# Performance work log

Hardware: AMD Instinct MI355X
Metric: run time of the kernel (lower is better)

Reference implementation:

```python
import jax, jax.numpy as jnp
import numpy as np

LOG2 = 0.6931471805599453  # shifted_softplus(x) = softplus(x) - log(2)
NUM_MOL = 20_000  # static maxm for segment reduction


def ssp(x):
    return jax.nn.softplus(x) - LOG2


def setup_inputs() -> dict:
    key = jax.random.key(0)
    ks = jax.random.split(key, 5)
    N, D, H, E, M = 1_000_000, 128, 64, 4, NUM_MOL
    x = jax.random.normal(ks[0], (N, D), dtype=jnp.float32)
    zidx = jax.random.randint(ks[1], (N,), 0, E, dtype=jnp.int32)
    idx_m = jnp.sort(jax.random.randint(ks[2], (N,), 0, M, dtype=jnp.int32))
    # stacked per-element pyramidal MLP params: D -> D//2 -> 1
    W1 = jax.random.normal(ks[3], (E, D, H), dtype=jnp.float32) * (1.0 / np.sqrt(D))
    b1 = jnp.zeros((E, H), dtype=jnp.float32)
    W2 = jax.random.normal(ks[4], (E, H, 1), dtype=jnp.float32) * (1.0 / np.sqrt(H))
    b2 = jnp.zeros((E, 1), dtype=jnp.float32)
    return dict(x=x, zidx=zidx, idx_m=idx_m, W1=W1, b1=b1, W2=W2, b2=b2)


def reference(x, zidx, idx_m, W1, b1, W2, b2):
    # ElementwiseMLP: run each element's 2-layer MLP, select per atom by element.
    E = W1.shape[0]
    yi = jnp.zeros((x.shape[0], W2.shape[-1]), dtype=x.dtype)  # [N, n_out]
    for e in range(E):  # small fixed element set
        h = ssp(x @ W1[e] + b1[e])            # [N, H]
        ye = h @ W2[e] + b2[e]                # [N, n_out]
        yi = yi + jnp.where((zidx == e)[:, None], ye, jnp.zeros((), dtype=x.dtype))
    # aggregation_mode == 'sum': index_add per molecule
    y = jax.ops.segment_sum(yi, idx_m, num_segments=NUM_MOL)  # [M, n_out]
    return jnp.squeeze(y, -1)  # [M]
```

## Files before the change

kernel.cpp:

```cpp
#include <hip/hip_runtime.h>

typedef _Float16 half8 __attribute__((ext_vector_type(8)));
typedef float f32x4 __attribute__((ext_vector_type(4)));

#define WS_COUNT(e)  ((e) * 32)
#define WS_AOFF(e)   (128 + (e))
#define WS_FILL(e)   (136 + (e))
#define WS_CUR(e)    (160 + (e) * 32)
#define WS_PERM      512

__global__ void k_count(const int* __restrict__ zidx, int N, int* __restrict__ ws) {
  __shared__ int lh[4];
  if (threadIdx.x < 4) lh[threadIdx.x] = 0;
  __syncthreads();
  const int i = blockIdx.x * 256 + threadIdx.x;
  const int z = (i < N) ? zidx[i] : -1;
  const int lane = threadIdx.x & 63;
#pragma unroll
  for (int e = 0; e < 4; ++e) {
    unsigned long long m = __ballot(z == e);
    if (lane == 0 && m) atomicAdd(&lh[e], __popcll(m));
  }
  __syncthreads();
  if (threadIdx.x < 4 && lh[threadIdx.x])
    atomicAdd(&ws[WS_COUNT(threadIdx.x)], lh[threadIdx.x]);
}

__global__ void k_offsets(int* __restrict__ ws) {
  if (threadIdx.x != 0) return;
  int off = 0;
#pragma unroll
  for (int e = 0; e < 4; ++e) {
    int c = ws[WS_COUNT(e)];
    ws[WS_AOFF(e)] = off;
    ws[WS_FILL(e)] = off + c;
    ws[WS_CUR(e)] = off;
    off += (c + 255) & ~255;
  }
  ws[WS_AOFF(4)] = off;
}

__global__ void k_scatter(const int* __restrict__ zidx, int N, int* __restrict__ ws) {
  __shared__ int wcnt[4][4];
  __shared__ int wbase[4][4];
  const int tid = threadIdx.x;
  const int lane = tid & 63;
  const int wave = tid >> 6;
  const int i = blockIdx.x * 256 + tid;
  const int z = (i < N) ? zidx[i] : -1;
  const unsigned long long m0 = __ballot(z == 0);
  const unsigned long long m1 = __ballot(z == 1);
  const unsigned long long m2 = __ballot(z == 2);
  const unsigned long long m3 = __ballot(z == 3);
  if (lane == 0) {
    wcnt[wave][0] = __popcll(m0);
    wcnt[wave][1] = __popcll(m1);
    wcnt[wave][2] = __popcll(m2);
    wcnt[wave][3] = __popcll(m3);
  }
  __syncthreads();
  if (tid < 4) {
    const int e = tid;
    const int c0 = wcnt[0][e], c1 = wcnt[1][e], c2 = wcnt[2][e], c3 = wcnt[3][e];
    const int base = atomicAdd(&ws[WS_CUR(e)], c0 + c1 + c2 + c3);
    wbase[0][e] = base;
    wbase[1][e] = base + c0;
    wbase[2][e] = base + c0 + c1;
    wbase[3][e] = base + c0 + c1 + c2;
  }
  __syncthreads();
  if (z >= 0) {
    const unsigned long long below = (1ull << lane) - 1ull;
    int r, b;
    if (z == 0)      { r = __popcll(m0 & below); b = wbase[wave][0]; }
    else if (z == 1) { r = __popcll(m1 & below); b = wbase[wave][1]; }
    else if (z == 2) { r = __popcll(m2 & below); b = wbase[wave][2]; }
    else             { r = __popcll(m3 & below); b = wbase[wave][3]; }
    ws[WS_PERM + b + r] = i;
  }
}

__global__ __launch_bounds__(256, 3)
void elemental_sorted_kernel(const float* __restrict__ x,
                             const int* __restrict__ idx_m,
                             const float* __restrict__ W1,
                             const float* __restrict__ b1,
                             const float* __restrict__ W2,
                             const float* __restrict__ b2,
                             const int* __restrict__ ws,
                             float* __restrict__ y) {
  __shared__ _Float16 w1t[8192];

  const int bstart = blockIdx.x << 8;
  if (bstart >= ws[WS_AOFF(4)]) return;
  int e = 0;
  if (bstart >= ws[WS_AOFF(1)]) e = 1;
  if (bstart >= ws[WS_AOFF(2)]) e = 2;
  if (bstart >= ws[WS_AOFF(3)]) e = 3;
  const int fillE = ws[WS_FILL(e)];

  const float* w1e = W1 + (size_t)e * 8192;
  const int tid = threadIdx.x;
#pragma unroll
  for (int t = 0; t < 4; ++t) {
    const int ch = tid + t * 256;
    const int kt = ch >> 8;
    const int nt = (ch >> 6) & 3;
    const int l2 = ch & 63;
    const int h = nt * 16 + (l2 & 15);
    const int d0 = kt * 32 + (l2 >> 4) * 8;
    half8 hv;
#pragma unroll
    for (int j = 0; j < 8; ++j)
      hv[j] = (_Float16)w1e[(d0 + j) * 64 + h];
    *(half8*)&w1t[ch * 8] = hv;
  }
  __syncthreads();

  const int lane = tid & 63;
  const int wave = tid >> 6;
  const int c = lane & 15;
  const int q = lane >> 4;
  const int pos = bstart + wave * 64 + lane;
  const int ap = (pos < fillE) ? ws[WS_PERM + pos] : -1;
  const int iv = (ap >= 0) ? idx_m[ap] : 0;

  half8 af[4][4];
#pragma unroll
  for (int mt = 0; mt < 4; ++mt) {
    int pa = __shfl(ap, mt * 16 + c);
    const f32x4* rp = (const f32x4*)(x + (long)(pa < 0 ? 0 : pa) * 128);
#pragma unroll
    for (int kt = 0; kt < 4; ++kt) {
      f32x4 u0 = rp[kt * 8 + q * 2];
      f32x4 u1 = rp[kt * 8 + q * 2 + 1];
      half8 a;
      a[0] = (_Float16)u0[0]; a[1] = (_Float16)u0[1];
      a[2] = (_Float16)u0[2]; a[3] = (_Float16)u0[3];
      a[4] = (_Float16)u1[0]; a[5] = (_Float16)u1[1];
      a[6] = (_Float16)u1[2]; a[7] = (_Float16)u1[3];
      af[mt][kt] = a;
    }
  }

  f32x4 acc[4][4];
#pragma unroll
  for (int mt = 0; mt < 4; ++mt)
#pragma unroll
    for (int nt = 0; nt < 4; ++nt)
      acc[mt][nt] = (f32x4){0.f, 0.f, 0.f, 0.f};

#pragma unroll
  for (int kt = 0; kt < 4; ++kt)
#pragma unroll
    for (int nt = 0; nt < 4; ++nt) {
      half8 bf = *(const half8*)&w1t[((kt * 4 + nt) * 64 + lane) * 8];
#pragma unroll
      for (int mt = 0; mt < 4; ++mt)
        acc[mt][nt] = __builtin_amdgcn_mfma_f32_16x16x32_f16(af[mt][kt], bf, acc[mt][nt], 0, 0, 0);
    }

  float b1v[4], w2v[4];
#pragma unroll
  for (int nt = 0; nt < 4; ++nt) {
    b1v[nt] = b1[e * 64 + nt * 16 + c];
    w2v[nt] = W2[e * 64 + nt * 16 + c];
  }
  const float b2e = b2[e];
#pragma unroll
  for (int mt = 0; mt < 4; ++mt) {
#pragma unroll
    for (int i = 0; i < 4; ++i) {
      float s = 0.0f;
#pragma unroll
      for (int nt = 0; nt < 4; ++nt) {
        float tv = acc[mt][nt][i] + b1v[nt];
        float hsp = __logf(1.0f + __expf(tv)) - 0.69314718056f;
        s = fmaf(hsp, w2v[nt], s);
      }
      s += __shfl_xor(s, 1);
      s += __shfl_xor(s, 2);
      s += __shfl_xor(s, 4);
      s += __shfl_xor(s, 8);
      const int mloc = mt * 16 + q * 4 + i;
      const int av = __shfl(ap, mloc);
      const int im = __shfl(iv, mloc);
      if (c == 0 && av >= 0)
        atomicAdd(&y[im], s + b2e);
    }
  }
}

#define LDSROW_OLD 136

__global__ __launch_bounds__(256, 2)
void elemental_atomwise_kernel(const float* __restrict__ x,
                               const int* __restrict__ zidx,
                               const int* __restrict__ idx_m,
                               const float* __restrict__ W1,
                               const float* __restrict__ b1,
                               const float* __restrict__ W2,
                               const float* __restrict__ b2,
                               float* __restrict__ y,
                               int N) {
  extern __shared__ _Float16 w1t[];
#pragma unroll
  for (int it = 0; it < 32; ++it) {
    int idx4 = threadIdx.x + it * 256;
    f32x4 v = ((const f32x4*)W1)[idx4];
    int lin = idx4 << 2;
    int d = (lin >> 6) & 127;
    int ee = lin >> 13;
    int h = lin & 63;
    int n = ee * 64 + h;
#pragma unroll
    for (int j = 0; j < 4; ++j)
      w1t[(n + j) * LDSROW_OLD + d] = (_Float16)v[j];
  }
  __syncthreads();

  const int lane = threadIdx.x & 63;
  const int wave = threadIdx.x >> 6;
  const int c = lane & 15;
  const int q = lane >> 4;
  const long tile = (long)blockIdx.x * 4 + wave;
  const long base = tile * 64;
  if (base >= N) return;

  int ameta = (base + lane < N) ? (int)(base + lane) : (N - 1);
  const int zvec = zidx[ameta];
  const int ivec = idx_m[ameta];

  half8 af[4][4];
#pragma unroll
  for (int mt = 0; mt < 4; ++mt) {
    long row = base + mt * 16 + c;
    if (row >= N) row = N - 1;
    const f32x4* rp = (const f32x4*)(x + row * 128);
#pragma unroll
    for (int kt = 0; kt < 4; ++kt) {
      f32x4 u0 = rp[kt * 8 + q * 2];
      f32x4 u1 = rp[kt * 8 + q * 2 + 1];
      half8 a;
      a[0] = (_Float16)u0[0]; a[1] = (_Float16)u0[1];
      a[2] = (_Float16)u0[2]; a[3] = (_Float16)u0[3];
      a[4] = (_Float16)u1[0]; a[5] = (_Float16)u1[1];
      a[6] = (_Float16)u1[2]; a[7] = (_Float16)u1[3];
      af[mt][kt] = a;
    }
  }

#pragma unroll
  for (int e = 0; e < 4; ++e) {
    f32x4 acc[4][4];
#pragma unroll
    for (int mt = 0; mt < 4; ++mt)
#pragma unroll
      for (int nt = 0; nt < 4; ++nt)
        acc[mt][nt] = (f32x4){0.f, 0.f, 0.f, 0.f};

#pragma unroll
    for (int kt = 0; kt < 4; ++kt) {
#pragma unroll
      for (int nt = 0; nt < 4; ++nt) {
        half8 bf = *(const half8*)&w1t[(e * 64 + nt * 16 + c) * LDSROW_OLD + kt * 32 + q * 8];
#pragma unroll
        for (int mt = 0; mt < 4; ++mt)
          acc[mt][nt] = __builtin_amdgcn_mfma_f32_16x16x32_f16(af[mt][kt], bf, acc[mt][nt], 0, 0, 0);
      }
    }

    float b1v[4], w2v[4];
#pragma unroll
    for (int nt = 0; nt < 4; ++nt) {
      b1v[nt] = b1[e * 64 + nt * 16 + c];
      w2v[nt] = W2[e * 64 + nt * 16 + c];
    }
    const float b2e = b2[e];
#pragma unroll
    for (int mt = 0; mt < 4; ++mt) {
#pragma unroll
      for (int i = 0; i < 4; ++i) {
        float s = 0.0f;
#pragma unroll
        for (int nt = 0; nt < 4; ++nt) {
          float tv = acc[mt][nt][i] + b1v[nt];
          float hsp = __logf(1.0f + __expf(tv)) - 0.69314718056f;
          s = fmaf(hsp, w2v[nt], s);
        }
        s += __shfl_xor(s, 1);
        s += __shfl_xor(s, 2);
        s += __shfl_xor(s, 4);
        s += __shfl_xor(s, 8);
        int mloc = mt * 16 + q * 4 + i;
        int zm = __shfl(zvec, mloc);
        int im = __shfl(ivec, mloc);
        if (c == 0 && zm == e && base + mloc < N)
          atomicAdd(&y[im], s + b2e);
      }
    }
  }
}

extern "C" void kernel_launch(void* const* d_in, const int* in_sizes, int n_in,
                              void* d_out, int out_size, void* d_ws, size_t ws_size,
                              hipStream_t stream) {
  const float* x = (const float*)d_in[0];
  const int* zidx = (const int*)d_in[1];
  const int* idx_m = (const int*)d_in[2];
  const float* W1 = (const float*)d_in[3];
  const float* b1 = (const float*)d_in[4];
  const float* W2 = (const float*)d_in[5];
  const float* b2 = (const float*)d_in[6];
  float* y = (float*)d_out;

  const int N = in_sizes[0] / 128;

  hipMemsetAsync(d_out, 0, (size_t)out_size * sizeof(float), stream);

  const size_t ws_need = (size_t)(WS_PERM + N + 1024) * sizeof(int);
  if (ws_size >= ws_need) {
    int* ws = (int*)d_ws;
    hipMemsetAsync(d_ws, 0, 1024, stream);
    const int nb = (N + 255) / 256;
    k_count<<<nb, 256, 0, stream>>>(zidx, N, ws);
    k_offsets<<<1, 64, 0, stream>>>(ws);
    k_scatter<<<nb, 256, 0, stream>>>(zidx, N, ws);
    const int nb4 = (N + 1020 + 255) / 256;
    elemental_sorted_kernel<<<nb4, 256, 0, stream>>>(x, idx_m, W1, b1, W2, b2, ws, y);
  } else {
    const int tiles = (N + 63) / 64;
    const int blocks = (tiles + 3) / 4;
    const size_t lds_bytes = 256 * LDSROW_OLD * sizeof(_Float16);
    elemental_atomwise_kernel<<<blocks, 256, lds_bytes, stream>>>(
        x, zidx, idx_m, W1, b1, W2, b2, y, N);
  }
}
```

Baseline: 779.9 us.

## Pre-convert W1 to fp16 once and shrink sorted kernel to 64-atom blocks

The per-element W1 fp16 conversion and MFMA-fragment swizzle move into the counting kernel, which writes them once to workspace. The sorted MLP kernel then does a straight vectorised copy into LDS instead of strided fp32 loads and conversions. Each wave now handles 16 atoms instead of 64, so each block covers 64 atoms. This cuts accumulator and fragment registers, raises the occupancy target, and gives more blocks in flight to hide the latency of the gathered x loads. In exchange, 16KB of W1 is copied into LDS per 64 atoms instead of per 256, which raises L2 and LDS traffic per atom.

```diff
diff --git a/kernel.cpp b/kernel.cpp
--- a/kernel.cpp
+++ b/kernel.cpp
@@ -9,7 +9,8 @@
 #define WS_CUR(e)    (160 + (e) * 32)
 #define WS_PERM      512
 
-__global__ void k_count(const int* __restrict__ zidx, int N, int* __restrict__ ws) {
+__global__ void k_count(const int* __restrict__ zidx, int N, int* __restrict__ ws,
+                        const float* __restrict__ W1, _Float16* __restrict__ w1h) {
   __shared__ int lh[4];
   if (threadIdx.x < 4) lh[threadIdx.x] = 0;
   __syncthreads();
@@ -20,6 +21,18 @@
   for (int e = 0; e < 4; ++e) {
     unsigned long long m = __ballot(z == e);
     if (lane == 0 && m) atomicAdd(&lh[e], __popcll(m));
+  }
+  if (blockIdx.x < 16) {
+    const int cg = blockIdx.x * 256 + threadIdx.x;
+    const int e = cg >> 10, ch = cg & 1023;
+    const int kt = ch >> 8, nt = (ch >> 6) & 3, l2 = ch & 63;
+    const int h = nt * 16 + (l2 & 15);
+    const int d0 = kt * 32 + (l2 >> 4) * 8;
+    const float* w1e = W1 + (size_t)e * 8192;
+    half8 hv;
+#pragma unroll
+    for (int j = 0; j < 8; ++j) hv[j] = (_Float16)w1e[(d0 + j) * 64 + h];
+    *(half8*)&w1h[(size_t)cg * 8] = hv;
   }
   __syncthreads();
   if (threadIdx.x < 4 && lh[threadIdx.x])
@@ -80,18 +93,18 @@
   }
 }
 
-__global__ __launch_bounds__(256, 3)
-void elemental_sorted_kernel(const float* __restrict__ x,
-                             const int* __restrict__ idx_m,
-                             const float* __restrict__ W1,
-                             const float* __restrict__ b1,
-                             const float* __restrict__ W2,
-                             const float* __restrict__ b2,
-                             const int* __restrict__ ws,
-                             float* __restrict__ y) {
+__global__ __launch_bounds__(256, 4)
+void elemental_sorted16(const float* __restrict__ x,
+                        const int* __restrict__ idx_m,
+                        const _Float16* __restrict__ w1h,
+                        const float* __restrict__ b1,
+                        const float* __restrict__ W2,
+                        const float* __restrict__ b2,
+                        const int* __restrict__ ws,
+                        float* __restrict__ y) {
   __shared__ _Float16 w1t[8192];
 
-  const int bstart = blockIdx.x << 8;
+  const int bstart = blockIdx.x * 64;
   if (bstart >= ws[WS_AOFF(4)]) return;
   int e = 0;
   if (bstart >= ws[WS_AOFF(1)]) e = 1;
@@ -99,21 +112,12 @@
   if (bstart >= ws[WS_AOFF(3)]) e = 3;
   const int fillE = ws[WS_FILL(e)];
 
-  const float* w1e = W1 + (size_t)e * 8192;
   const int tid = threadIdx.x;
-#pragma unroll
-  for (int t = 0; t < 4; ++t) {
-    const int ch = tid + t * 256;
-    const int kt = ch >> 8;
-    const int nt = (ch >> 6) & 3;
-    const int l2 = ch & 63;
-    const int h = nt * 16 + (l2 & 15);
-    const int d0 = kt * 32 + (l2 >> 4) * 8;
-    half8 hv;
-#pragma unroll
-    for (int j = 0; j < 8; ++j)
-      hv[j] = (_Float16)w1e[(d0 + j) * 64 + h];
-    *(half8*)&w1t[ch * 8] = hv;
+  const half8* src = (const half8*)w1h + (size_t)e * 1024;
+#pragma unroll
+  for (int it = 0; it < 4; ++it) {
+    const int kk = it * 256 + tid;
+    *(half8*)&w1t[kk * 8] = src[kk];
   }
   __syncthreads();
 
@@ -121,43 +125,33 @@
   const int wave = tid >> 6;
   const int c = lane & 15;
   const int q = lane >> 4;
-  const int pos = bstart + wave * 64 + lane;
+  const int pos = bstart + wave * 16 + c;
   const int ap = (pos < fillE) ? ws[WS_PERM + pos] : -1;
   const int iv = (ap >= 0) ? idx_m[ap] : 0;
 
-  half8 af[4][4];
-#pragma unroll
-  for (int mt = 0; mt < 4; ++mt) {
-    int pa = __shfl(ap, mt * 16 + c);
-    const f32x4* rp = (const f32x4*)(x + (long)(pa < 0 ? 0 : pa) * 128);
-#pragma unroll
-    for (int kt = 0; kt < 4; ++kt) {
-      f32x4 u0 = rp[kt * 8 + q * 2];
-      f32x4 u1 = rp[kt * 8 + q * 2 + 1];
-      half8 a;
-      a[0] = (_Float16)u0[0]; a[1] = (_Float16)u0[1];
-      a[2] = (_Float16)u0[2]; a[3] = (_Float16)u0[3];
-      a[4] = (_Float16)u1[0]; a[5] = (_Float16)u1[1];
-      a[6] = (_Float16)u1[2]; a[7] = (_Float16)u1[3];
-      af[mt][kt] = a;
-    }
-  }
-
-  f32x4 acc[4][4];
-#pragma unroll
-  for (int mt = 0; mt < 4; ++mt)
-#pragma unroll
-    for (int nt = 0; nt < 4; ++nt)
-      acc[mt][nt] = (f32x4){0.f, 0.f, 0.f, 0.f};
-
+  const f32x4* rp = (const f32x4*)(x + (long)(ap < 0 ? 0 : ap) * 128);
+  half8 af[4];
+#pragma unroll
+  for (int kt = 0; kt < 4; ++kt) {
+    f32x4 u0 = rp[kt * 8 + q * 2];
+    f32x4 u1 = rp[kt * 8 + q * 2 + 1];
+    half8 a;
+    a[0] = (_Float16)u0[0]; a[1] = (_Float16)u0[1];
+    a[2] = (_Float16)u0[2]; a[3] = (_Float16)u0[3];
+    a[4] = (_Float16)u1[0]; a[5] = (_Float16)u1[1];
+    a[6] = (_Float16)u1[2]; a[7] = (_Float16)u1[3];
+    af[kt] = a;
+  }
+
+  f32x4 acc[4];
+#pragma unroll
+  for (int nt = 0; nt < 4; ++nt) acc[nt] = (f32x4){0.f, 0.f, 0.f, 0.f};
 #pragma unroll
   for (int kt = 0; kt < 4; ++kt)
 #pragma unroll
     for (int nt = 0; nt < 4; ++nt) {
       half8 bf = *(const half8*)&w1t[((kt * 4 + nt) * 64 + lane) * 8];
-#pragma unroll
-      for (int mt = 0; mt < 4; ++mt)
-        acc[mt][nt] = __builtin_amdgcn_mfma_f32_16x16x32_f16(af[mt][kt], bf, acc[mt][nt], 0, 0, 0);
+      acc[nt] = __builtin_amdgcn_mfma_f32_16x16x32_f16(af[kt], bf, acc[nt], 0, 0, 0);
     }
 
   float b1v[4], w2v[4];
@@ -168,26 +162,23 @@
   }
   const float b2e = b2[e];
 #pragma unroll
-  for (int mt = 0; mt < 4; ++mt) {
-#pragma unroll
-    for (int i = 0; i < 4; ++i) {
-      float s = 0.0f;
-#pragma unroll
-      for (int nt = 0; nt < 4; ++nt) {
-        float tv = acc[mt][nt][i] + b1v[nt];
-        float hsp = __logf(1.0f + __expf(tv)) - 0.69314718056f;
-        s = fmaf(hsp, w2v[nt], s);
-      }
-      s += __shfl_xor(s, 1);
-      s += __shfl_xor(s, 2);
-      s += __shfl_xor(s, 4);
-      s += __shfl_xor(s, 8);
-      const int mloc = mt * 16 + q * 4 + i;
-      const int av = __shfl(ap, mloc);
-      const int im = __shfl(iv, mloc);
-      if (c == 0 && av >= 0)
-        atomicAdd(&y[im], s + b2e);
-    }
+  for (int i = 0; i < 4; ++i) {
+    float s = 0.0f;
+#pragma unroll
+    for (int nt = 0; nt < 4; ++nt) {
+      float tv = acc[nt][i] + b1v[nt];
+      float hsp = __logf(1.0f + __expf(tv)) - 0.69314718056f;
+      s = fmaf(hsp, w2v[nt], s);
+    }
+    s += __shfl_xor(s, 1);
+    s += __shfl_xor(s, 2);
+    s += __shfl_xor(s, 4);
+    s += __shfl_xor(s, 8);
+    const int slot = q * 4 + i;
+    const int av = __shfl(ap, slot);
+    const int im = __shfl(iv, slot);
+    if (c == 0 && av >= 0)
+      atomicAdd(&y[im], s + b2e);
   }
 }
 
@@ -318,16 +309,19 @@
 
   hipMemsetAsync(d_out, 0, (size_t)out_size * sizeof(float), stream);
 
-  const size_t ws_need = (size_t)(WS_PERM + N + 1024) * sizeof(int);
+  const int w1h_off = (512 + N + 1024 + 3) & ~3;
+  const size_t ws_need = (size_t)w1h_off * sizeof(int) + 65536;
   if (ws_size >= ws_need) {
     int* ws = (int*)d_ws;
+    _Float16* w1h = (_Float16*)(ws + w1h_off);
     hipMemsetAsync(d_ws, 0, 1024, stream);
     const int nb = (N + 255) / 256;
-    k_count<<<nb, 256, 0, stream>>>(zidx, N, ws);
+    const int nbc = nb < 16 ? 16 : nb;
+    k_count<<<nbc, 256, 0, stream>>>(zidx, N, ws, W1, w1h);
     k_offsets<<<1, 64, 0, stream>>>(ws);
     k_scatter<<<nb, 256, 0, stream>>>(zidx, N, ws);
-    const int nb4 = (N + 1020 + 255) / 256;
-    elemental_sorted_kernel<<<nb4, 256, 0, stream>>>(x, idx_m, W1, b1, W2, b2, ws, y);
+    const int nb64 = (N + 1020 + 63) / 64;
+    elemental_sorted16<<<nb64, 256, 0, stream>>>(x, idx_m, w1h, b1, W2, b2, ws, y);
   } else {
     const int tiles = (N + 63) / 64;
     const int blocks = (tiles + 3) / 4;
```

Measured after the change: 768.5 us. No clear change (-1.5%).
